# Kernel optimization log

Measured on AMD Instinct MI355X. Metric: run time of the kernel, lower is better.

## Reference

```python
import jax, jax.numpy as jnp
import numpy as np

D_MODEL = 1024
NUM_HEADS = 16
D_HEAD = D_MODEL // NUM_HEADS
B, T = 2, 2048


def setup_inputs() -> dict:
    key = jax.random.key(0)
    k1, k2, k3 = jax.random.split(key, 3)
    std_qkv = np.sqrt(2.0 / (3 * D_MODEL + D_MODEL))
    std_out = np.sqrt(2.0 / (D_MODEL + D_MODEL))
    x = jax.random.normal(k1, (B, T, D_MODEL), dtype=jnp.float32)
    Wqkv = jax.random.normal(k2, (3 * D_MODEL, D_MODEL), dtype=jnp.float32) * std_qkv
    Wout = jax.random.normal(k3, (D_MODEL, D_MODEL), dtype=jnp.float32) * std_out
    return {"x": x, "Wqkv": Wqkv, "Wout": Wout}


def reference(x, Wqkv, Wout):
    Bz, Tz, _ = x.shape
    qkv = jnp.einsum('btd,ed->bte', x, Wqkv)  # [B,T,3*d_model]
    q, k, v = jnp.split(qkv, 3, axis=-1)
    # [B,T,H,Dh] -> [B,H,T,Dh]
    def to_heads(t):
        return t.reshape(Bz, Tz, NUM_HEADS, D_HEAD).transpose(0, 2, 1, 3)
    q, k, v = to_heads(q), to_heads(k), to_heads(v)
    scale = 1.0 / jnp.sqrt(jnp.asarray(D_HEAD, dtype=x.dtype))
    scores = jnp.einsum('bhqd,bhkd->bhqk', q, k) * scale
    causal = jnp.tril(jnp.ones((Tz, Tz), dtype=bool))
    scores = jnp.where(causal, scores, -jnp.inf)
    weights = jax.nn.softmax(scores, axis=-1)
    y = jnp.einsum('bhqk,bhkd->bhqd', weights, v)
    y = y.transpose(0, 2, 1, 3).reshape(Bz, Tz, D_MODEL)
    return jnp.einsum('btd,ed->bte', y, Wout)
```

## Files before the change

kernel.cpp:

```cpp
#include <hip/hip_runtime.h>
#include <hip/hip_bf16.h>

#define B_SZ    2
#define T_SEQ   2048
#define D_MODEL 1024
#define N_HEADS 16
#define D_HEAD  64
#define BT      (B_SZ * T_SEQ)

typedef unsigned short u16;
typedef __attribute__((ext_vector_type(8))) short  short8;
typedef __attribute__((ext_vector_type(4))) float  floatx4;
typedef __attribute__((ext_vector_type(4))) unsigned short ushortx4;

__device__ inline u16 f2b(float f) {
    __hip_bfloat16 h = __float2bfloat16(f);
    return *(u16*)&h;
}

__device__ inline void gld_lds16(const void* g, void* l) {
    __builtin_amdgcn_global_load_lds(
        (const __attribute__((address_space(1))) void*)g,
        (__attribute__((address_space(3))) void*)l, 16, 0, 0);
}

__global__ __launch_bounds__(256) void cvt3_kernel(
    const float* __restrict__ x, const float* __restrict__ wq,
    const float* __restrict__ wo,
    u16* __restrict__ xb, u16* __restrict__ wqb, u16* __restrict__ wob)
{
    const int n4x = (BT * D_MODEL) / 4;
    const int n4q = (3 * D_MODEL * D_MODEL) / 4;
    const int n4o = (D_MODEL * D_MODEL) / 4;
    int i = blockIdx.x * 256 + threadIdx.x;
    const float* src; u16* dst;
    if (i < n4x)            { src = x;  dst = xb;  }
    else if (i < n4x + n4q) { i -= n4x; src = wq; dst = wqb; }
    else                    { i -= n4x + n4q; if (i >= n4o) return; src = wo; dst = wob; }
    floatx4 v = ((const floatx4*)src)[i];
    ushortx4 r;
    r[0] = f2b(v[0]); r[1] = f2b(v[1]); r[2] = f2b(v[2]); r[3] = f2b(v[3]);
    ((ushortx4*)dst)[i] = r;
}

__global__ __launch_bounds__(256) void gemm_qkv_kernel(
    const u16* __restrict__ A, const u16* __restrict__ B,
    u16* __restrict__ Qb, u16* __restrict__ Kb, u16* __restrict__ Vt)
{
    const int K = D_MODEL;
    __shared__ __align__(16) u16 Ab[128][32];
    __shared__ __align__(16) u16 Bb[128][32];
    __shared__ __align__(16) u16 Tb[4][64][72];

    const int tid  = threadIdx.x;
    const int w    = tid >> 6;
    const int lane = tid & 63;
    const int col  = lane & 15;
    const int quad = lane >> 4;
    const int wm   = w & 1;
    const int wn   = w >> 1;

    const int tm = blockIdx.x & 31;
    const int tn = blockIdx.x >> 5;

    const int r0 = w * 32;
    const int lr = lane >> 2;
    const int ls = (lane & 3) << 3;
    const u16* gA0 = A + (size_t)(tm * 128 + r0 + lr) * K + ls;
    const u16* gA1 = gA0 + (size_t)16 * K;
    const u16* gB0 = B + (size_t)(tn * 128 + r0 + lr) * K + ls;
    const u16* gB1 = gB0 + (size_t)16 * K;
    u16* lA0 = &Ab[r0][0];
    u16* lA1 = &Ab[r0 + 16][0];
    u16* lB0 = &Bb[r0][0];
    u16* lB1 = &Bb[r0 + 16][0];

    floatx4 acc[4][4];
    #pragma unroll
    for (int i = 0; i < 4; ++i)
        #pragma unroll
        for (int j = 0; j < 4; ++j) acc[i][j] = (floatx4){0.f, 0.f, 0.f, 0.f};

    for (int k0 = 0; k0 < K; k0 += 32) {
        __syncthreads();
        gld_lds16(gA0 + k0, lA0);
        gld_lds16(gA1 + k0, lA1);
        gld_lds16(gB0 + k0, lB0);
        gld_lds16(gB1 + k0, lB1);
        __syncthreads();

        short8 af[4], bf[4];
        #pragma unroll
        for (int mt = 0; mt < 4; ++mt)
            af[mt] = *(const short8*)&Ab[wm * 64 + mt * 16 + col][quad * 8];
        #pragma unroll
        for (int nt = 0; nt < 4; ++nt)
            bf[nt] = *(const short8*)&Bb[wn * 64 + nt * 16 + col][quad * 8];
        #pragma unroll
        for (int mt = 0; mt < 4; ++mt)
            #pragma unroll
            for (int nt = 0; nt < 4; ++nt)
                acc[mt][nt] = __builtin_amdgcn_mfma_f32_16x16x32_bf16(
                    af[mt], bf[nt], acc[mt][nt], 0, 0, 0);
    }

    if (tn < 16) {
        #pragma unroll
        for (int nt = 0; nt < 4; ++nt) {
            const int gcol = tn * 128 + wn * 64 + nt * 16 + col;
            const int sec = gcol >> 10;
            const int h   = (gcol >> 6) & 15;
            const int d   = gcol & 63;
            #pragma unroll
            for (int mt = 0; mt < 4; ++mt) {
                #pragma unroll
                for (int rr = 0; rr < 4; ++rr) {
                    const int m  = tm * 128 + wm * 64 + mt * 16 + quad * 4 + rr;
                    const int bb = m >> 11;
                    const int tl = m & (T_SEQ - 1);
                    const float v = acc[mt][nt][rr];
                    if (sec == 0)
                        Qb[((size_t)(bb * N_HEADS + h) * T_SEQ + tl) * D_HEAD + d] = f2b(v * 0.125f);
                    else
                        Kb[((size_t)(bb * N_HEADS + h) * T_SEQ + tl) * D_HEAD + d] = f2b(v);
                }
            }
        }
    } else {
        #pragma unroll
        for (int nt = 0; nt < 4; ++nt)
            #pragma unroll
            for (int mt = 0; mt < 4; ++mt) {
                ushortx4 pk;
                pk[0] = f2b(acc[mt][nt][0]); pk[1] = f2b(acc[mt][nt][1]);
                pk[2] = f2b(acc[mt][nt][2]); pk[3] = f2b(acc[mt][nt][3]);
                *(ushortx4*)&Tb[w][nt * 16 + col][mt * 16 + quad * 4] = pk;
            }
        const int vcol0 = (tn - 16) * 128 + wn * 64;
        const int bb    = tm >> 4;
        const int tg0   = (tm & 15) * 128 + wm * 64 + ((lane & 7) << 3);
        #pragma unroll
        for (int j = 0; j < 8; ++j) {
            const int d_loc = j * 8 + (lane >> 3);
            const int vcol  = vcol0 + d_loc;
            const int h     = vcol >> 6;
            const int d     = vcol & 63;
            short8 row = *(const short8*)&Tb[w][d_loc][(lane & 7) << 3];
            *(short8*)(Vt + ((size_t)(bb * N_HEADS + h) * D_HEAD + d) * T_SEQ + tg0) = row;
        }
    }
}

__global__ __launch_bounds__(256) void gemm_out_kernel(
    const u16* __restrict__ A, const u16* __restrict__ B, float* __restrict__ C)
{
    const int K = D_MODEL, N = D_MODEL;
    __shared__ __align__(16) u16 Ab[64][32];
    __shared__ __align__(16) u16 Bb[128][32];

    const int tid  = threadIdx.x;
    const int w    = tid >> 6;
    const int lane = tid & 63;
    const int col  = lane & 15;
    const int quad = lane >> 4;

    const int tm = blockIdx.x & 63;
    const int tn = blockIdx.x >> 6;

    const int lr = lane >> 2;
    const int ls = (lane & 3) << 3;
    const u16* gA  = A + (size_t)(tm * 64 + w * 16 + lr) * K + ls;
    const u16* gB0 = B + (size_t)(tn * 128 + w * 32 + lr) * K + ls;
    const u16* gB1 = gB0 + (size_t)16 * K;
    u16* lA  = &Ab[w * 16][0];
    u16* lB0 = &Bb[w * 32][0];
    u16* lB1 = &Bb[w * 32 + 16][0];

    floatx4 acc[4][2];
    #pragma unroll
    for (int i = 0; i < 4; ++i) {
        acc[i][0] = (floatx4){0.f, 0.f, 0.f, 0.f};
        acc[i][1] = (floatx4){0.f, 0.f, 0.f, 0.f};
    }

    for (int k0 = 0; k0 < K; k0 += 32) {
        __syncthreads();
        gld_lds16(gA + k0, lA);
        gld_lds16(gB0 + k0, lB0);
        gld_lds16(gB1 + k0, lB1);
        __syncthreads();

        short8 af[4], bf[2];
        #pragma unroll
        for (int mt = 0; mt < 4; ++mt)
            af[mt] = *(const short8*)&Ab[mt * 16 + col][quad * 8];
        #pragma unroll
        for (int nt = 0; nt < 2; ++nt)
            bf[nt] = *(const short8*)&Bb[w * 32 + nt * 16 + col][quad * 8];
        #pragma unroll
        for (int mt = 0; mt < 4; ++mt)
            #pragma unroll
            for (int nt = 0; nt < 2; ++nt)
                acc[mt][nt] = __builtin_amdgcn_mfma_f32_16x16x32_bf16(
                    af[mt], bf[nt], acc[mt][nt], 0, 0, 0);
    }

    #pragma unroll
    for (int nt = 0; nt < 2; ++nt) {
        const int gcol = tn * 128 + w * 32 + nt * 16 + col;
        #pragma unroll
        for (int mt = 0; mt < 4; ++mt)
            #pragma unroll
            for (int rr = 0; rr < 4; ++rr) {
                const int m = tm * 64 + mt * 16 + quad * 4 + rr;
                C[(size_t)m * N + gcol] = acc[mt][nt][rr];
            }
    }
}

__global__ __launch_bounds__(256) void attn_mfma_kernel(
    const u16* __restrict__ Qb, const u16* __restrict__ Kb,
    const u16* __restrict__ Vt, u16* __restrict__ y)
{
    const int bid = blockIdx.x;
    const int qt  = 31 - (bid >> 5);
    const int bh  = bid & 31;
    const int b   = bh >> 4;
    const int h   = bh & 15;

    __shared__ __align__(16) u16 KV[2][2][64][64];
    __shared__ __align__(16) u16 Pl[4][16][64];

    const int tid  = threadIdx.x;
    const int w    = tid >> 6;
    const int lane = tid & 63;
    const int col  = lane & 15;
    const int quad = lane >> 4;

    const int srl  = lane >> 3;
    const int sseg = ((lane & 7) ^ srl) << 3;
    const int row0 = w * 16 + srl;
    const u16* kbase = Kb + (size_t)bh * T_SEQ * D_HEAD;
    const u16* vbase = Vt + (size_t)bh * D_HEAD * T_SEQ;
    const size_t offK0 = (size_t)row0 * D_HEAD + sseg;
    const size_t offK1 = offK0 + (size_t)8 * D_HEAD;
    const size_t offV0 = (size_t)row0 * T_SEQ + sseg;
    const size_t offV1 = offV0 + (size_t)8 * T_SEQ;

    short8 qf0, qf1;
    {
        const u16* qp = Qb + ((size_t)(bh * T_SEQ + qt * 64 + w * 16 + col)) * D_HEAD + quad * 8;
        qf0 = *(const short8*)qp;
        qf1 = *(const short8*)(qp + 32);
    }

    float l_s = 0.f;
    floatx4 O[4];
    #pragma unroll
    for (int dt = 0; dt < 4; ++dt) O[dt] = (floatx4){0.f, 0.f, 0.f, 0.f};

    const int c7 = col & 7;
    const int sA = (quad ^ c7) << 3;
    const int sB = ((quad ^ c7) ^ 4) << 3;

    u16* const plrow = &Pl[w][col][0];
    int pwoff[4], proff[2];
    #pragma unroll
    for (int ct = 0; ct < 4; ++ct)
        pwoff[ct] = (((ct * 2 + (quad >> 1)) ^ c7) << 3) + ((quad & 1) << 2);
    #pragma unroll
    for (int c = 0; c < 2; ++c)
        proff[c] = ((c * 4 + quad) ^ c7) << 3;

    gld_lds16(kbase + offK0, &KV[0][0][w * 16][0]);
    gld_lds16(kbase + offK1, &KV[0][0][w * 16 + 8][0]);
    gld_lds16(vbase + offV0, &KV[0][1][w * 16][0]);
    gld_lds16(vbase + offV1, &KV[0][1][w * 16 + 8][0]);

    for (int kt = 0; kt <= qt; ++kt) {
        __syncthreads();

        if (kt < qt) {
            const int nb = (kt + 1) & 1;
            const u16* kt_k = kbase + (size_t)(kt + 1) * 64 * D_HEAD;
            const u16* kt_v = vbase + (size_t)(kt + 1) * 64;
            gld_lds16(kt_k + offK0, &KV[nb][0][w * 16][0]);
            gld_lds16(kt_k + offK1, &KV[nb][0][w * 16 + 8][0]);
            gld_lds16(kt_v + offV0, &KV[nb][1][w * 16][0]);
            gld_lds16(kt_v + offV1, &KV[nb][1][w * 16 + 8][0]);
        }

        const u16 (*Ksb)[64] = KV[kt & 1][0];
        const u16 (*Vsb)[64] = KV[kt & 1][1];

        const bool diag  = (kt == qt);
        const int  ctmax = diag ? w : 3;

        #pragma unroll
        for (int ct = 0; ct < 4; ++ct) {
            ushortx4 pk;
            if (ct <= ctmax) {
                const u16* kp = &Ksb[ct * 16 + col][0];
                short8 k0 = *(const short8*)(kp + sA);
                short8 k1 = *(const short8*)(kp + sB);
                floatx4 acc = {0.f, 0.f, 0.f, 0.f};
                acc = __builtin_amdgcn_mfma_f32_16x16x32_bf16(k0, qf0, acc, 0, 0, 0);
                acc = __builtin_amdgcn_mfma_f32_16x16x32_bf16(k1, qf1, acc, 0, 0, 0);
                if (diag && ct == ctmax) {
                    #pragma unroll
                    for (int r = 0; r < 4; ++r)
                        if (quad * 4 + r > col) acc[r] = -1e30f;
                }
                #pragma unroll
                for (int r = 0; r < 4; ++r) {
                    const float p = __expf(acc[r]);
                    l_s += p;
                    pk[r] = f2b(p);
                }
            } else {
                pk[0] = pk[1] = pk[2] = pk[3] = 0;
            }
            *(ushortx4*)(plrow + pwoff[ct]) = pk;
        }

        const int kchunks = diag ? ((ctmax * 16 + 15) >> 5) : 1;
        #pragma unroll
        for (int c = 0; c < 2; ++c) {
            if (c <= kchunks) {
                short8 pa = *(const short8*)(plrow + proff[c]);
                #pragma unroll
                for (int dt = 0; dt < 4; ++dt) {
                    const u16* vp = &Vsb[dt * 16 + col][0];
                    short8 vb = *(const short8*)(vp + (c ? sB : sA));
                    O[dt] = __builtin_amdgcn_mfma_f32_16x16x32_bf16(pa, vb, O[dt], 0, 0, 0);
                }
            }
        }
    }

    l_s += __shfl_xor(l_s, 16);
    l_s += __shfl_xor(l_s, 32);
    float inv_row[4];
    #pragma unroll
    for (int r = 0; r < 4; ++r) inv_row[r] = 1.0f / __shfl(l_s, quad * 4 + r);
    #pragma unroll
    for (int dt = 0; dt < 4; ++dt)
        #pragma unroll
        for (int r = 0; r < 4; ++r) {
            const size_t q_g = (size_t)(b * T_SEQ + qt * 64 + w * 16 + quad * 4 + r);
            y[q_g * D_MODEL + h * D_HEAD + dt * 16 + col] = f2b(O[dt][r] * inv_row[r]);
        }
}

extern "C" void kernel_launch(void* const* d_in, const int* in_sizes, int n_in,
                              void* d_out, int out_size, void* d_ws, size_t ws_size,
                              hipStream_t stream) {
    const float* x    = (const float*)d_in[0];
    const float* Wqkv = (const float*)d_in[1];
    const float* Wout = (const float*)d_in[2];
    float* out = (float*)d_out;

    u16* xb    = (u16*)d_ws;
    u16* wqkvb = (u16*)((char*)d_ws + ( 8u << 20));
    u16* woutb = (u16*)((char*)d_ws + (14u << 20));
    u16* Qb    = (u16*)((char*)d_ws + (16u << 20));
    u16* Kb    = (u16*)((char*)d_ws + (24u << 20));
    u16* Vtb   = (u16*)((char*)d_ws + (32u << 20));
    u16* yb    = (u16*)((char*)d_ws + (40u << 20));

    cvt3_kernel<<<8192, 256, 0, stream>>>(x, Wqkv, Wout, xb, wqkvb, woutb);

    gemm_qkv_kernel<<<32 * (3 * D_MODEL / 128), 256, 0, stream>>>(
        xb, wqkvb, Qb, Kb, Vtb);

    attn_mfma_kernel<<<B_SZ * N_HEADS * (T_SEQ / 64), 256, 0, stream>>>(
        Qb, Kb, Vtb, yb);

    gemm_out_kernel<<<512, 256, 0, stream>>>(yb, woutb, out);
}
```

Before: 167.0 us.

## Process 128 query rows per attention block to reuse K/V tiles

Each block now covers 128 query rows, with each wave handling two 16-row groups, instead of 64 rows. Every K/V tile loaded into LDS is therefore used by twice as many queries, which halves the number of blocks and the K/V global traffic per query. In exchange, each wave holds more registers (two accumulator sets), the grid shrinks to 512 blocks, and causal-diagonal masking now wastes more work at tile granularity.

```diff
diff --git a/kernel.cpp b/kernel.cpp
--- a/kernel.cpp
+++ b/kernel.cpp
@@ -223,13 +223,15 @@
     const u16* __restrict__ Vt, u16* __restrict__ y)
 {
     const int bid = blockIdx.x;
-    const int qt  = 31 - (bid >> 5);
     const int bh  = bid & 31;
+    const int i   = 15 - (bid >> 5);
+    const int qb  = i * 128;
+    const int kt1 = 2 * i + 2;
     const int b   = bh >> 4;
     const int h   = bh & 15;
 
     __shared__ __align__(16) u16 KV[2][2][64][64];
-    __shared__ __align__(16) u16 Pl[4][16][64];
+    __shared__ __align__(16) u16 Pl[4][32][64];
 
     const int tid  = threadIdx.x;
     const int w    = tid >> 6;
@@ -247,23 +249,25 @@
     const size_t offV0 = (size_t)row0 * T_SEQ + sseg;
     const size_t offV1 = offV0 + (size_t)8 * T_SEQ;
 
-    short8 qf0, qf1;
-    {
-        const u16* qp = Qb + ((size_t)(bh * T_SEQ + qt * 64 + w * 16 + col)) * D_HEAD + quad * 8;
-        qf0 = *(const short8*)qp;
-        qf1 = *(const short8*)(qp + 32);
-    }
-
-    float l_s = 0.f;
-    floatx4 O[4];
-    #pragma unroll
-    for (int dt = 0; dt < 4; ++dt) O[dt] = (floatx4){0.f, 0.f, 0.f, 0.f};
+    short8 qf[2][2];
+    #pragma unroll
+    for (int g = 0; g < 2; ++g) {
+        const u16* qp = Qb + ((size_t)(bh * T_SEQ + qb + w * 32 + g * 16 + col)) * D_HEAD + quad * 8;
+        qf[g][0] = *(const short8*)qp;
+        qf[g][1] = *(const short8*)(qp + 32);
+    }
+
+    float l_s[2] = {0.f, 0.f};
+    floatx4 O[2][4];
+    #pragma unroll
+    for (int g = 0; g < 2; ++g)
+        #pragma unroll
+        for (int dt = 0; dt < 4; ++dt) O[g][dt] = (floatx4){0.f, 0.f, 0.f, 0.f};
 
     const int c7 = col & 7;
     const int sA = (quad ^ c7) << 3;
     const int sB = ((quad ^ c7) ^ 4) << 3;
 
-    u16* const plrow = &Pl[w][col][0];
     int pwoff[4], proff[2];
     #pragma unroll
     for (int ct = 0; ct < 4; ++ct)
@@ -271,16 +275,19 @@
     #pragma unroll
     for (int c = 0; c < 2; ++c)
         proff[c] = ((c * 4 + quad) ^ c7) << 3;
+
+    const int qbw0 = qb + w * 32;
+    const int qbw1 = qbw0 + 16;
 
     gld_lds16(kbase + offK0, &KV[0][0][w * 16][0]);
     gld_lds16(kbase + offK1, &KV[0][0][w * 16 + 8][0]);
     gld_lds16(vbase + offV0, &KV[0][1][w * 16][0]);
     gld_lds16(vbase + offV1, &KV[0][1][w * 16 + 8][0]);
 
-    for (int kt = 0; kt <= qt; ++kt) {
-        __syncthreads();
-
-        if (kt < qt) {
+    for (int kt = 0; kt < kt1; ++kt) {
+        __syncthreads();
+
+        if (kt + 1 < kt1) {
             const int nb = (kt + 1) & 1;
             const u16* kt_k = kbase + (size_t)(kt + 1) * 64 * D_HEAD;
             const u16* kt_v = vbase + (size_t)(kt + 1) * 64;
@@ -293,63 +300,73 @@
         const u16 (*Ksb)[64] = KV[kt & 1][0];
         const u16 (*Vsb)[64] = KV[kt & 1][1];
 
-        const bool diag  = (kt == qt);
-        const int  ctmax = diag ? w : 3;
-
         #pragma unroll
         for (int ct = 0; ct < 4; ++ct) {
-            ushortx4 pk;
-            if (ct <= ctmax) {
+            const int kg = kt * 64 + ct * 16;
+            short8 k0, k1;
+            if (kg <= qbw1) {
                 const u16* kp = &Ksb[ct * 16 + col][0];
-                short8 k0 = *(const short8*)(kp + sA);
-                short8 k1 = *(const short8*)(kp + sB);
-                floatx4 acc = {0.f, 0.f, 0.f, 0.f};
-                acc = __builtin_amdgcn_mfma_f32_16x16x32_bf16(k0, qf0, acc, 0, 0, 0);
-                acc = __builtin_amdgcn_mfma_f32_16x16x32_bf16(k1, qf1, acc, 0, 0, 0);
-                if (diag && ct == ctmax) {
+                k0 = *(const short8*)(kp + sA);
+                k1 = *(const short8*)(kp + sB);
+            }
+            #pragma unroll
+            for (int g = 0; g < 2; ++g) {
+                const int qbg = g ? qbw1 : qbw0;
+                ushortx4 pk;
+                if (kg <= qbg) {
+                    floatx4 acc = {0.f, 0.f, 0.f, 0.f};
+                    acc = __builtin_amdgcn_mfma_f32_16x16x32_bf16(k0, qf[g][0], acc, 0, 0, 0);
+                    acc = __builtin_amdgcn_mfma_f32_16x16x32_bf16(k1, qf[g][1], acc, 0, 0, 0);
+                    if (kg == qbg) {
+                        #pragma unroll
+                        for (int r = 0; r < 4; ++r)
+                            if (quad * 4 + r > col) acc[r] = -1e30f;
+                    }
                     #pragma unroll
-                    for (int r = 0; r < 4; ++r)
-                        if (quad * 4 + r > col) acc[r] = -1e30f;
+                    for (int r = 0; r < 4; ++r) {
+                        const float p = __expf(acc[r]);
+                        l_s[g] += p;
+                        pk[r] = f2b(p);
+                    }
+                } else {
+                    pk[0] = pk[1] = pk[2] = pk[3] = 0;
                 }
-                #pragma unroll
-                for (int r = 0; r < 4; ++r) {
-                    const float p = __expf(acc[r]);
-                    l_s += p;
-                    pk[r] = f2b(p);
-                }
-            } else {
-                pk[0] = pk[1] = pk[2] = pk[3] = 0;
-            }
-            *(ushortx4*)(plrow + pwoff[ct]) = pk;
-        }
-
-        const int kchunks = diag ? ((ctmax * 16 + 15) >> 5) : 1;
+                *(ushortx4*)(&Pl[w][g * 16 + col][0] + pwoff[ct]) = pk;
+            }
+        }
+
         #pragma unroll
         for (int c = 0; c < 2; ++c) {
-            if (c <= kchunks) {
-                short8 pa = *(const short8*)(plrow + proff[c]);
+            if (kt * 64 + c * 32 <= qbw1 + 15) {
+                short8 pa0 = *(const short8*)(&Pl[w][col][0] + proff[c]);
+                short8 pa1 = *(const short8*)(&Pl[w][16 + col][0] + proff[c]);
                 #pragma unroll
                 for (int dt = 0; dt < 4; ++dt) {
                     const u16* vp = &Vsb[dt * 16 + col][0];
                     short8 vb = *(const short8*)(vp + (c ? sB : sA));
-                    O[dt] = __builtin_amdgcn_mfma_f32_16x16x32_bf16(pa, vb, O[dt], 0, 0, 0);
+                    O[0][dt] = __builtin_amdgcn_mfma_f32_16x16x32_bf16(pa0, vb, O[0][dt], 0, 0, 0);
+                    O[1][dt] = __builtin_amdgcn_mfma_f32_16x16x32_bf16(pa1, vb, O[1][dt], 0, 0, 0);
                 }
             }
         }
     }
 
-    l_s += __shfl_xor(l_s, 16);
-    l_s += __shfl_xor(l_s, 32);
-    float inv_row[4];
-    #pragma unroll
-    for (int r = 0; r < 4; ++r) inv_row[r] = 1.0f / __shfl(l_s, quad * 4 + r);
-    #pragma unroll
-    for (int dt = 0; dt < 4; ++dt)
-        #pragma unroll
-        for (int r = 0; r < 4; ++r) {
-            const size_t q_g = (size_t)(b * T_SEQ + qt * 64 + w * 16 + quad * 4 + r);
-            y[q_g * D_MODEL + h * D_HEAD + dt * 16 + col] = f2b(O[dt][r] * inv_row[r]);
-        }
+    #pragma unroll
+    for (int g = 0; g < 2; ++g) {
+        float l = l_s[g];
+        l += __shfl_xor(l, 16);
+        l += __shfl_xor(l, 32);
+        float inv_row[4];
+        #pragma unroll
+        for (int r = 0; r < 4; ++r) inv_row[r] = 1.0f / __shfl(l, quad * 4 + r);
+        #pragma unroll
+        for (int dt = 0; dt < 4; ++dt)
+            #pragma unroll
+            for (int r = 0; r < 4; ++r) {
+                const size_t q_g = (size_t)(b * T_SEQ + qb + w * 32 + g * 16 + quad * 4 + r);
+                y[q_g * D_MODEL + h * D_HEAD + dt * 16 + col] = f2b(O[g][dt][r] * inv_row[r]);
+            }
+    }
 }
 
 extern "C" void kernel_launch(void* const* d_in, const int* in_sizes, int n_in,
@@ -373,8 +390,7 @@
     gemm_qkv_kernel<<<32 * (3 * D_MODEL / 128), 256, 0, stream>>>(
         xb, wqkvb, Qb, Kb, Vtb);
 
-    attn_mfma_kernel<<<B_SZ * N_HEADS * (T_SEQ / 64), 256, 0, stream>>>(
-        Qb, Kb, Vtb, yb);
+    attn_mfma_kernel<<<512, 256, 0, stream>>>(Qb, Kb, Vtb, yb);
 
     gemm_out_kernel<<<512, 256, 0, stream>>>(yb, woutb, out);
 }
```

New measurement: 191.3 us. 14.5% more time.
